# Kernel optimization log

Hardware: AMD Instinct MI355X
Metric: run time of the kernel (lower is better)

## Reference

```python
import jax, jax.numpy as jnp
import numpy as np

HIST_LEN = 100  # STDP history cap in the original module


def setup_inputs() -> dict:
    key = jax.random.key(0)
    ks = jax.random.split(key, 5)
    H, B = 1024, 16384
    return {
        "x": jax.random.normal(ks[0], (B, H), dtype=jnp.float32),
        "weights": jax.random.normal(ks[1], (H, H), dtype=jnp.float32) * 0.1,
        "meta_plasticity": jnp.ones((H,), dtype=jnp.float32),
        "pre_hist": jax.random.normal(ks[2], (HIST_LEN, H), dtype=jnp.float32) * 0.1,
        "post_hist": jax.random.normal(ks[3], (HIST_LEN, H), dtype=jnp.float32) * 0.1,
        "activity_history": jnp.zeros((1000,), dtype=jnp.float32),
        "history_pointer": 5,
        "stdp_window": jnp.float32(20.0),
        "stdp_decay": jnp.float32(0.1),
        "target_activity": jnp.float32(0.1),
        "homeostatic_rate": jnp.float32(0.01),
        "meta_learning_rate": jnp.float32(0.001),
    }


def reference(x, weights, meta_plasticity, pre_hist, post_hist,
              activity_history, history_pointer, stdp_window, stdp_decay,
              target_activity, homeostatic_rate, meta_learning_rate):
    # --- forward matmul: weights * meta_plasticity scales columns (broadcast over rows)
    output = x @ (weights * meta_plasticity)  # [B, H]

    # --- STDP update (vectorized form of the python loop over the history) ---
    # append current mean activities, pop oldest (steady-state length == HIST_LEN)
    pre = jnp.concatenate([pre_hist[1:], x.mean(axis=0)[None]], axis=0)       # [L, H]
    post = jnp.concatenate([post_hist[1:], output.mean(axis=0)[None]], axis=0)
    L = HIST_LEN
    i = jnp.arange(L, dtype=jnp.float32)
    dt = (L - i) * stdp_window
    w = 0.01 * jnp.exp(-dt * stdp_decay)                                      # [L]
    pos_w = jnp.where(i < L - 1, w, 0.0)   # i < len-1 branch
    neg_w = jnp.where(i > 0, w, 0.0)       # i > 0 branch
    # sum_i pos_w[i] * outer(post[-1], pre[i]) = outer(post[-1], pos_w @ pre)
    dW = jnp.outer(post[-1], pos_w @ pre) - jnp.outer(neg_w @ post, pre[-1])
    new_w = jnp.clip(weights + dW, -1.0, 1.0)

    # --- homeostatic plasticity ---
    hist = activity_history.at[history_pointer].set(output.mean())
    activity_diff = target_activity - hist.mean()
    new_w = jnp.clip(new_w * (1.0 + homeostatic_rate * activity_diff), -1.0, 1.0)

    # --- meta plasticity ---
    new_meta = jnp.clip(
        meta_plasticity + meta_learning_rate * (output.mean(axis=0) - meta_plasticity),
        0.0, 2.0)

    return output, new_w, new_meta, hist
```

## Files before the change

kernel.cpp:

```cpp
#include <hip/hip_runtime.h>
#include <hip/hip_bf16.h>

#define H 1024
#define BATCH 16384

typedef unsigned short u16;
typedef u16 u16x8 __attribute__((ext_vector_type(8)));
typedef __bf16 bf16x8 __attribute__((ext_vector_type(8)));
typedef float f32x4 __attribute__((ext_vector_type(4)));

typedef __attribute__((address_space(3))) unsigned int lds_uint;
typedef __attribute__((address_space(1))) const unsigned int glob_uint;

__device__ __forceinline__ u16 f2bf(float f) {
  unsigned int u = __float_as_uint(f);
  u += 0x7fffu + ((u >> 16) & 1u);
  return (u16)(u >> 16);
}

#define WS_XSUMP   0
#define WS_XSUM    (WS_XSUMP + 256 * H)
#define WS_ORAWP   (WS_XSUM + H)
#define WS_POSVP   (WS_ORAWP + 16 * H)
#define WS_NEGHP   (WS_POSVP + 5 * H)
#define WS_SCRATCH (WS_NEGHP + 5 * H)
#define WS_BF16    (WS_SCRATCH + 16)

__global__ __launch_bounds__(256) void prep_kernel(const float* __restrict__ X,
                                                   const float* __restrict__ W,
                                                   u16* __restrict__ Xb,
                                                   u16* __restrict__ Wbt,
                                                   float* __restrict__ ws,
                                                   const float* __restrict__ pre,
                                                   const float* __restrict__ post,
                                                   const float* __restrict__ win,
                                                   const float* __restrict__ dec) {
  __shared__ __align__(16) u16 t[64][72];
  const int b = blockIdx.x, tid = threadIdx.x;
  if (b < 256) {
    size_t r0 = (size_t)b * 64;
    float s0 = 0.f, s1 = 0.f, s2 = 0.f, s3 = 0.f;
#pragma unroll 4
    for (int r = 0; r < 64; ++r) {
      size_t off = (r0 + r) * H + tid * 4;
      const float4 v = *(const float4*)&X[off];
      ushort4 h;
      h.x = f2bf(v.x); h.y = f2bf(v.y); h.z = f2bf(v.z); h.w = f2bf(v.w);
      *(ushort4*)&Xb[off] = h;
      s0 += v.x; s1 += v.y; s2 += v.z; s3 += v.w;
    }
    float* row = &ws[WS_XSUMP + b * H];
    row[tid * 4 + 0] = s0; row[tid * 4 + 1] = s1;
    row[tid * 4 + 2] = s2; row[tid * 4 + 3] = s3;
  } else if (b < 512) {
    const int b2 = b - 256;
    const int n0 = (b2 & 15) * 64, k0 = (b2 >> 4) * 64;
    const int rb = tid >> 4, c4 = tid & 15;
#pragma unroll
    for (int i = 0; i < 4; ++i) {
      int r = rb + i * 16;
      const float4 v = *(const float4*)&W[(size_t)(k0 + r) * H + n0 + c4 * 4];
      t[c4 * 4 + 0][r] = f2bf(v.x);
      t[c4 * 4 + 1][r] = f2bf(v.y);
      t[c4 * 4 + 2][r] = f2bf(v.z);
      t[c4 * 4 + 3][r] = f2bf(v.w);
    }
    __syncthreads();
    const int seg = tid & 7;
#pragma unroll
    for (int p = 0; p < 2; ++p) {
      int wr = p * 32 + (tid >> 3);
      *(u16x8*)&Wbt[(size_t)(n0 + wr) * H + k0 + seg * 8] = *(const u16x8*)&t[wr][seg * 8];
    }
  } else {
    const int b2 = b - 512;
    const int col = (b2 & 3) * 256 + tid;
    const int seg = b2 >> 2;
    const int t0 = 1 + seg * 20;
    int tend = t0 + 20; if (tend > 100) tend = 100;
    float wd = win[0] * dec[0];
    float ps = 0.f, ns = 0.f;
    for (int tt = t0; tt < tend; ++tt) {
      float w = 0.01f * expf(-(float)(101 - tt) * wd);
      ps += w * pre[tt * H + col];
      if (tt >= 2) ns += w * post[tt * H + col];
    }
    ws[WS_POSVP + seg * H + col] = ps;
    ws[WS_NEGHP + seg * H + col] = ns;
  }
}

__global__ __launch_bounds__(256) void gemm_vm_kernel(const u16* __restrict__ Xb,
                                                      const u16* __restrict__ Wbt,
                                                      const float* __restrict__ meta,
                                                      const float* __restrict__ W,
                                                      float* __restrict__ ws,
                                                      float* __restrict__ out) {
  __shared__ __align__(16) u16 lA[128 * 32];
  __shared__ __align__(16) u16 lB[128 * 32];
  __shared__ float xs[64];

  const int b = blockIdx.x, tid = threadIdx.x;

  if (b < 64) {
    const int jx = b & 3, ky = b >> 2;
    if (tid < 64) {
      float s = 0.f;
      const float* p = &ws[WS_XSUMP + ky * 64 + tid];
#pragma unroll 8
      for (int q = 0; q < 256; ++q) s += p[q * H];
      xs[tid] = s;
      if (jx == 0) ws[WS_XSUM + ky * 64 + tid] = s;
    }
    __syncthreads();
    const int j = jx * 256 + tid;
    float s = 0.f;
#pragma unroll 8
    for (int k = 0; k < 64; ++k) s += xs[k] * W[(size_t)(ky * 64 + k) * H + j];
    ws[WS_ORAWP + ky * H + j] = s * (1.0f / (float)BATCH);
    return;
  }

  const int bg = b - 64;
  const int mt = bg & 127, nt = bg >> 7;
  const size_t row0 = (size_t)mt * 128;
  const int col0 = nt * 128;
  const int wave = tid >> 6;
  const int lane = tid & 63;
  const int quad = lane >> 4;
  const int l16 = lane & 15;
  const int wm = wave >> 1, wn = wave & 1;

  const int sr = lane >> 2;
  const int sk = (lane & 3) * 8;

  f32x4 acc[4][4];
#pragma unroll
  for (int i = 0; i < 4; ++i)
#pragma unroll
    for (int j = 0; j < 4; ++j) acc[i][j] = (f32x4){0.f, 0.f, 0.f, 0.f};

  for (int k0 = 0; k0 < H; k0 += 32) {
#pragma unroll
    for (int i = 0; i < 2; ++i) {
      const int rg = i * 64 + wave * 16;
      const u16* ga = &Xb[(row0 + rg + sr) * H + k0 + sk];
      const u16* gb = &Wbt[(size_t)(col0 + rg + sr) * H + k0 + sk];
      __builtin_amdgcn_global_load_lds((glob_uint*)ga, (lds_uint*)&lA[rg * 32], 16, 0, 0);
      __builtin_amdgcn_global_load_lds((glob_uint*)gb, (lds_uint*)&lB[rg * 32], 16, 0, 0);
    }
    __syncthreads();

    bf16x8 av[4], bv[4];
#pragma unroll
    for (int f = 0; f < 4; ++f) {
      av[f] = __builtin_bit_cast(bf16x8, *(const u16x8*)&lA[(wm * 64 + f * 16 + l16) * 32 + quad * 8]);
      bv[f] = __builtin_bit_cast(bf16x8, *(const u16x8*)&lB[(wn * 64 + f * 16 + l16) * 32 + quad * 8]);
    }
#pragma unroll
    for (int fm = 0; fm < 4; ++fm)
#pragma unroll
      for (int fn = 0; fn < 4; ++fn)
        acc[fm][fn] = __builtin_amdgcn_mfma_f32_16x16x32_bf16(av[fm], bv[fn], acc[fm][fn], 0, 0, 0);
    __syncthreads();
  }

  float mcol[4];
#pragma unroll
  for (int fn = 0; fn < 4; ++fn) mcol[fn] = meta[col0 + wn * 64 + fn * 16 + l16];
#pragma unroll
  for (int fm = 0; fm < 4; ++fm) {
#pragma unroll
    for (int fn = 0; fn < 4; ++fn) {
      int col = col0 + wn * 64 + fn * 16 + l16;
#pragma unroll
      for (int r = 0; r < 4; ++r) {
        size_t row = row0 + wm * 64 + fm * 16 + quad * 4 + r;
        out[row * H + col] = acc[fm][fn][r] * mcol[fn];
      }
    }
  }
}

__global__ __launch_bounds__(256) void tail_kernel(const float* __restrict__ W,
                                                   const float* __restrict__ meta,
                                                   const float* __restrict__ act,
                                                   const int* __restrict__ ptr,
                                                   const float* __restrict__ targ,
                                                   const float* __restrict__ homeo,
                                                   const float* __restrict__ mlr,
                                                   const float* __restrict__ win,
                                                   const float* __restrict__ dec,
                                                   const float* __restrict__ ws,
                                                   float* __restrict__ out_w,
                                                   float* __restrict__ meta_out,
                                                   float* __restrict__ hist_out) {
  __shared__ float r1[4], r2[4];
  const int r = blockIdx.x;
  const int t = threadIdx.x;
  const int c4 = t * 4;

  f32x4 oraw = (f32x4){0.f, 0.f, 0.f, 0.f};
#pragma unroll
  for (int i = 0; i < 16; ++i) {
    const float4 v = *(const float4*)&ws[WS_ORAWP + i * H + c4];
    oraw[0] += v.x; oraw[1] += v.y; oraw[2] += v.z; oraw[3] += v.w;
  }
  const float4 mv = *(const float4*)&meta[c4];
  f32x4 om;
  om[0] = mv.x * oraw[0]; om[1] = mv.y * oraw[1];
  om[2] = mv.z * oraw[2]; om[3] = mv.w * oraw[3];

  float s1 = om[0] + om[1] + om[2] + om[3];
  float s2 = 0.f;
#pragma unroll
  for (int j = 0; j < 4; ++j) {
    int idx = t + j * 256;
    if (idx < 1000) s2 += act[idx];
  }
#pragma unroll
  for (int o = 32; o > 0; o >>= 1) {
    s1 += __shfl_down(s1, o, 64);
    s2 += __shfl_down(s2, o, 64);
  }
  if ((t & 63) == 0) { r1[t >> 6] = s1; r2[t >> 6] = s2; }
  __syncthreads();
  const float ts1 = r1[0] + r1[1] + r1[2] + r1[3];
  const float ts2 = r2[0] + r2[1] + r2[2] + r2[3];
  const float total_mean = ts1 / (float)H;
  const int p = ptr[0];
  const float hist_mean = (ts2 - act[p] + total_mean) / 1000.f;
  const float scale = 1.f + homeo[0] * (targ[0] - hist_mean);
  const float w99 = 0.01f * expf(-win[0] * dec[0]);

  float oraw_r = 0.f;
#pragma unroll
  for (int i = 0; i < 16; ++i) oraw_r += ws[WS_ORAWP + i * H + r];
  const float om_r = meta[r] * oraw_r;
  float negh_r = 0.f;
#pragma unroll
  for (int i = 0; i < 5; ++i) negh_r += ws[WS_NEGHP + i * H + r];
  const float neg_r = negh_r + w99 * om_r;

  f32x4 pv = (f32x4){0.f, 0.f, 0.f, 0.f};
#pragma unroll
  for (int i = 0; i < 5; ++i) {
    const float4 v = *(const float4*)&ws[WS_POSVP + i * H + c4];
    pv[0] += v.x; pv[1] += v.y; pv[2] += v.z; pv[3] += v.w;
  }
  const float4 xv = *(const float4*)&ws[WS_XSUM + c4];
  float xx[4] = {xv.x, xv.y, xv.z, xv.w};
  const float4 wv = *(const float4*)&W[(size_t)r * H + c4];
  float wx[4] = {wv.x, wv.y, wv.z, wv.w};
  float4 o;
  float ox[4];
#pragma unroll
  for (int i = 0; i < 4; ++i) {
    float v = wx[i] + om_r * pv[i] - neg_r * (xx[i] * (1.0f / (float)BATCH));
    v = fminf(fmaxf(v, -1.f), 1.f);
    v = v * scale;
    ox[i] = fminf(fmaxf(v, -1.f), 1.f);
  }
  o.x = ox[0]; o.y = ox[1]; o.z = ox[2]; o.w = ox[3];
  *(float4*)&out_w[(size_t)r * H + c4] = o;

  if (r == 0) {
    float4 nm;
    float nx[4] = {mv.x, mv.y, mv.z, mv.w};
    float nr[4];
#pragma unroll
    for (int i = 0; i < 4; ++i) {
      float v = nx[i] + mlr[0] * (om[i] - nx[i]);
      nr[i] = fminf(fmaxf(v, 0.f), 2.f);
    }
    nm.x = nr[0]; nm.y = nr[1]; nm.z = nr[2]; nm.w = nr[3];
    *(float4*)&meta_out[c4] = nm;
#pragma unroll
    for (int j = 0; j < 4; ++j) {
      int idx = t + j * 256;
      if (idx < 1000) hist_out[idx] = (idx == p) ? total_mean : act[idx];
    }
  }
}

__global__ __launch_bounds__(256) void colsum_kernel(const float* __restrict__ x,
                                                     float* __restrict__ xsum) {
  int col = blockIdx.x * 256 + threadIdx.x;
  size_t r0 = (size_t)blockIdx.y * 256;
  float s = 0.f;
#pragma unroll 8
  for (int r = 0; r < 256; ++r) s += x[(r0 + r) * H + col];
  atomicAdd(&xsum[col], s);
}

__global__ __launch_bounds__(256) void gemm_fallback_kernel(const float* __restrict__ X,
                                                            const float* __restrict__ W,
                                                            const float* __restrict__ meta,
                                                            float* __restrict__ out) {
  __shared__ __align__(16) u16 lA[128][40];
  __shared__ __align__(16) u16 lB[128][40];
  const int tid = threadIdx.x;
  const int wave = tid >> 6;
  const int lane = tid & 63;
  const int quad = lane >> 4;
  const int l16 = lane & 15;
  const int wm = wave >> 1, wn = wave & 1;
  const size_t row0 = (size_t)blockIdx.x * 128;
  const int col0 = blockIdx.y * 128;
  f32x4 acc[4][4];
#pragma unroll
  for (int i = 0; i < 4; ++i)
#pragma unroll
    for (int j = 0; j < 4; ++j) acc[i][j] = (f32x4){0.f, 0.f, 0.f, 0.f};
  for (int k0 = 0; k0 < H; k0 += 32) {
#pragma unroll
    for (int i = 0; i < 4; ++i) {
      int idx = i * 256 + tid;
      int r = idx >> 3, c4 = idx & 7;
      const float4 v = *(const float4*)&X[(row0 + r) * H + k0 + c4 * 4];
      ushort4 h;
      h.x = f2bf(v.x); h.y = f2bf(v.y); h.z = f2bf(v.z); h.w = f2bf(v.w);
      *(ushort4*)&lA[r][c4 * 4] = h;
    }
#pragma unroll
    for (int i = 0; i < 4; ++i) {
      int idx = i * 256 + tid;
      int kk = idx >> 5, c4 = idx & 31;
      const float4 v = *(const float4*)&W[(size_t)(k0 + kk) * H + col0 + c4 * 4];
      lB[c4 * 4 + 0][kk] = f2bf(v.x);
      lB[c4 * 4 + 1][kk] = f2bf(v.y);
      lB[c4 * 4 + 2][kk] = f2bf(v.z);
      lB[c4 * 4 + 3][kk] = f2bf(v.w);
    }
    __syncthreads();
    bf16x8 av[4], bv[4];
#pragma unroll
    for (int f = 0; f < 4; ++f) {
      av[f] = __builtin_bit_cast(bf16x8, *(const u16x8*)&lA[wm * 64 + f * 16 + l16][quad * 8]);
      bv[f] = __builtin_bit_cast(bf16x8, *(const u16x8*)&lB[wn * 64 + f * 16 + l16][quad * 8]);
    }
#pragma unroll
    for (int fm = 0; fm < 4; ++fm)
#pragma unroll
      for (int fn = 0; fn < 4; ++fn)
        acc[fm][fn] = __builtin_amdgcn_mfma_f32_16x16x32_bf16(av[fm], bv[fn], acc[fm][fn], 0, 0, 0);
    __syncthreads();
  }
  float mcol[4];
#pragma unroll
  for (int fn = 0; fn < 4; ++fn) mcol[fn] = meta[col0 + wn * 64 + fn * 16 + l16];
#pragma unroll
  for (int fm = 0; fm < 4; ++fm) {
#pragma unroll
    for (int fn = 0; fn < 4; ++fn) {
      int col = col0 + wn * 64 + fn * 16 + l16;
#pragma unroll
      for (int r = 0; r < 4; ++r) {
        size_t row = row0 + wm * 64 + fm * 16 + quad * 4 + r;
        out[row * H + col] = acc[fm][fn][r] * mcol[fn];
      }
    }
  }
}

__global__ __launch_bounds__(256) void vecmat_kernel(const float* __restrict__ W,
                                                     const float* __restrict__ xsum,
                                                     float* __restrict__ outraw) {
  int j = blockIdx.x * 256 + threadIdx.x;
  int k0 = blockIdx.y * 64;
  float s = 0.f;
#pragma unroll 8
  for (int k = 0; k < 64; ++k) s += xsum[k0 + k] * W[(size_t)(k0 + k) * H + j];
  atomicAdd(&outraw[j], s * (1.0f / (float)BATCH));
}

__global__ __launch_bounds__(256) void stdpvec_kernel(const float* __restrict__ pre,
                                                      const float* __restrict__ post,
                                                      const float* __restrict__ win,
                                                      const float* __restrict__ dec,
                                                      float* __restrict__ posv,
                                                      float* __restrict__ negh) {
  int col = blockIdx.x * 256 + threadIdx.x;
  int t0 = 1 + blockIdx.y * 20;
  float wd = win[0] * dec[0];
  float ps = 0.f, ns = 0.f;
  int tend = t0 + 20;
  if (tend > 100) tend = 100;
  for (int t = t0; t < tend; ++t) {
    float w = 0.01f * expf(-(float)(101 - t) * wd);
    ps += w * pre[t * H + col];
    if (t >= 2) ns += w * post[t * H + col];
  }
  atomicAdd(&posv[col], ps);
  atomicAdd(&negh[col], ns);
}

__global__ __launch_bounds__(1024) void finalize_kernel(const float* __restrict__ meta,
                                                        const float* __restrict__ act,
                                                        const int* __restrict__ ptr,
                                                        const float* __restrict__ targ,
                                                        const float* __restrict__ homeo,
                                                        const float* __restrict__ mlr,
                                                        const float* __restrict__ outraw,
                                                        float* __restrict__ outmean,
                                                        float* __restrict__ scalep,
                                                        float* __restrict__ meta_out,
                                                        float* __restrict__ hist_out) {
  __shared__ float r1[16], r2[16];
  __shared__ float sc[2];
  int t = threadIdx.x;
  float om = meta[t] * outraw[t];
  outmean[t] = om;
  float a = (t < 1000) ? act[t] : 0.f;
  float s1 = om, s2 = a;
#pragma unroll
  for (int o = 32; o > 0; o >>= 1) {
    s1 += __shfl_down(s1, o, 64);
    s2 += __shfl_down(s2, o, 64);
  }
  if ((t & 63) == 0) { r1[t >> 6] = s1; r2[t >> 6] = s2; }
  __syncthreads();
  if (t == 0) {
    float ts1 = 0.f, ts2 = 0.f;
#pragma unroll
    for (int i = 0; i < 16; ++i) { ts1 += r1[i]; ts2 += r2[i]; }
    float total_mean = ts1 / (float)H;
    int p = ptr[0];
    float hist_mean = (ts2 - act[p] + total_mean) / 1000.f;
    float diff = targ[0] - hist_mean;
    sc[0] = 1.f + homeo[0] * diff;
    sc[1] = total_mean;
    scalep[0] = sc[0];
  }
  __syncthreads();
  float nm = meta[t] + mlr[0] * (om - meta[t]);
  nm = fminf(fmaxf(nm, 0.f), 2.f);
  meta_out[t] = nm;
  if (t < 1000) hist_out[t] = (t == ptr[0]) ? sc[1] : act[t];
}

__global__ __launch_bounds__(256) void neww_kernel(const float* __restrict__ W,
                                                   const float* __restrict__ outmean,
                                                   const float* __restrict__ posv,
                                                   const float* __restrict__ negh,
                                                   const float* __restrict__ xsum,
                                                   const float* __restrict__ scalep,
                                                   const float* __restrict__ win,
                                                   const float* __restrict__ dec,
                                                   float* __restrict__ out) {
  int idx4 = blockIdx.x * 256 + threadIdx.x;
  int rr = idx4 >> 8;
  int c4 = (idx4 & 255) * 4;
  float w99 = 0.01f * expf(-win[0] * dec[0]);
  float scale = scalep[0];
  float om_r = outmean[rr];
  float neg_r = negh[rr] + w99 * om_r;
  const float4 wv = *(const float4*)&W[(size_t)rr * H + c4];
  const float4 pv = *(const float4*)&posv[c4];
  const float4 xv = *(const float4*)&xsum[c4];
  float4 o;
  float vx[4] = {wv.x, wv.y, wv.z, wv.w};
  float px[4] = {pv.x, pv.y, pv.z, pv.w};
  float xx[4] = {xv.x, xv.y, xv.z, xv.w};
  float ox[4];
#pragma unroll
  for (int i = 0; i < 4; ++i) {
    float v = vx[i] + om_r * px[i] - neg_r * (xx[i] * (1.0f / (float)BATCH));
    v = fminf(fmaxf(v, -1.f), 1.f);
    v = v * scale;
    ox[i] = fminf(fmaxf(v, -1.f), 1.f);
  }
  o.x = ox[0]; o.y = ox[1]; o.z = ox[2]; o.w = ox[3];
  *(float4*)&out[(size_t)rr * H + c4] = o;
}

extern "C" void kernel_launch(void* const* d_in, const int* in_sizes, int n_in,
                              void* d_out, int out_size, void* d_ws, size_t ws_size,
                              hipStream_t stream) {
  const float* x     = (const float*)d_in[0];
  const float* W     = (const float*)d_in[1];
  const float* meta  = (const float*)d_in[2];
  const float* pre   = (const float*)d_in[3];
  const float* post  = (const float*)d_in[4];
  const float* act   = (const float*)d_in[5];
  const int*   ptr   = (const int*)d_in[6];
  const float* win   = (const float*)d_in[7];
  const float* dec   = (const float*)d_in[8];
  const float* targ  = (const float*)d_in[9];
  const float* homeo = (const float*)d_in[10];
  const float* mlr   = (const float*)d_in[11];

  float* out_y    = (float*)d_out;
  float* out_w    = out_y + (size_t)BATCH * H;
  float* out_meta = out_w + (size_t)H * H;
  float* out_hist = out_meta + H;

  float* ws = (float*)d_ws;
  u16* Xb  = (u16*)(ws + WS_BF16);
  u16* Wbt = Xb + (size_t)BATCH * H;

  const size_t ws_need = (size_t)WS_BF16 * sizeof(float) +
                         ((size_t)BATCH * H + (size_t)H * H) * sizeof(u16);

  if (ws_size >= ws_need) {
    prep_kernel<<<532, 256, 0, stream>>>(x, W, Xb, Wbt, ws, pre, post, win, dec);
    gemm_vm_kernel<<<1088, 256, 0, stream>>>(Xb, Wbt, meta, W, ws, out_y);
    tail_kernel<<<1024, 256, 0, stream>>>(W, meta, act, ptr, targ, homeo, mlr,
                                          win, dec, ws, out_w, out_meta, out_hist);
  } else {
    float* xsum    = ws;
    float* outraw  = ws + 1024;
    float* outmean = ws + 2048;
    float* posv    = ws + 3072;
    float* negh    = ws + 4096;
    float* scalep  = ws + 5120;
    hipMemsetAsync(d_ws, 0, 6144 * sizeof(float), stream);
    colsum_kernel<<<dim3(4, 64), 256, 0, stream>>>(x, xsum);
    gemm_fallback_kernel<<<dim3(128, 8), 256, 0, stream>>>(x, W, meta, out_y);
    vecmat_kernel<<<dim3(4, 16), 256, 0, stream>>>(W, xsum, outraw);
    stdpvec_kernel<<<dim3(4, 5), 256, 0, stream>>>(pre, post, win, dec, posv, negh);
    finalize_kernel<<<1, 1024, 0, stream>>>(meta, act, ptr, targ, homeo, mlr,
                                            outraw, outmean, scalep, out_meta, out_hist);
    neww_kernel<<<1024, 256, 0, stream>>>(W, outmean, posv, negh, xsum, scalep, win, dec, out_w);
  }
}
```

Measured before the change: 215.0 us.

## Double-buffer GEMM LDS tiles with XOR swizzle and MFMA priority boost

```diff
diff --git a/kernel.cpp b/kernel.cpp
--- a/kernel.cpp
+++ b/kernel.cpp
@@ -96,8 +96,8 @@
                                                       const float* __restrict__ W,
                                                       float* __restrict__ ws,
                                                       float* __restrict__ out) {
-  __shared__ __align__(16) u16 lA[128 * 32];
-  __shared__ __align__(16) u16 lB[128 * 32];
+  __shared__ __align__(16) u16 lA[2][128 * 32];
+  __shared__ __align__(16) u16 lB[2][128 * 32];
   __shared__ float xs[64];
 
   const int b = blockIdx.x, tid = threadIdx.x;
@@ -132,7 +132,8 @@
   const int wm = wave >> 1, wn = wave & 1;
 
   const int sr = lane >> 2;
-  const int sk = (lane & 3) * 8;
+  const int sk = (((lane & 3) ^ ((sr >> 1) & 3)) * 8);
+  const int ksw = ((quad ^ ((l16 >> 1) & 3)) * 8);
 
   f32x4 acc[4][4];
 #pragma unroll
@@ -140,29 +141,48 @@
 #pragma unroll
     for (int j = 0; j < 4; ++j) acc[i][j] = (f32x4){0.f, 0.f, 0.f, 0.f};
 
-  for (int k0 = 0; k0 < H; k0 += 32) {
-#pragma unroll
-    for (int i = 0; i < 2; ++i) {
-      const int rg = i * 64 + wave * 16;
-      const u16* ga = &Xb[(row0 + rg + sr) * H + k0 + sk];
-      const u16* gb = &Wbt[(size_t)(col0 + rg + sr) * H + k0 + sk];
-      __builtin_amdgcn_global_load_lds((glob_uint*)ga, (lds_uint*)&lA[rg * 32], 16, 0, 0);
-      __builtin_amdgcn_global_load_lds((glob_uint*)gb, (lds_uint*)&lB[rg * 32], 16, 0, 0);
-    }
-    __syncthreads();
+#pragma unroll
+  for (int i = 0; i < 2; ++i) {
+    const int rg = i * 64 + wave * 16;
+    const u16* ga = &Xb[(row0 + rg + sr) * H + 0 + sk];
+    const u16* gb = &Wbt[(size_t)(col0 + rg + sr) * H + 0 + sk];
+    __builtin_amdgcn_global_load_lds((glob_uint*)ga, (lds_uint*)&lA[0][rg * 32], 16, 0, 0);
+    __builtin_amdgcn_global_load_lds((glob_uint*)gb, (lds_uint*)&lB[0][rg * 32], 16, 0, 0);
+  }
+
+  for (int kt = 0; kt < 32; ++kt) {
+    const int cur = kt & 1;
+    if (kt < 31) {
+      const int k0n = (kt + 1) * 32;
+#pragma unroll
+      for (int i = 0; i < 2; ++i) {
+        const int rg = i * 64 + wave * 16;
+        const u16* ga = &Xb[(row0 + rg + sr) * H + k0n + sk];
+        const u16* gb = &Wbt[(size_t)(col0 + rg + sr) * H + k0n + sk];
+        __builtin_amdgcn_global_load_lds((glob_uint*)ga, (lds_uint*)&lA[cur ^ 1][rg * 32], 16, 0, 0);
+        __builtin_amdgcn_global_load_lds((glob_uint*)gb, (lds_uint*)&lB[cur ^ 1][rg * 32], 16, 0, 0);
+      }
+      asm volatile("s_waitcnt vmcnt(4)" ::: "memory");
+    } else {
+      asm volatile("s_waitcnt vmcnt(0)" ::: "memory");
+    }
+    asm volatile("s_barrier" ::: "memory");
 
     bf16x8 av[4], bv[4];
 #pragma unroll
     for (int f = 0; f < 4; ++f) {
-      av[f] = __builtin_bit_cast(bf16x8, *(const u16x8*)&lA[(wm * 64 + f * 16 + l16) * 32 + quad * 8]);
-      bv[f] = __builtin_bit_cast(bf16x8, *(const u16x8*)&lB[(wn * 64 + f * 16 + l16) * 32 + quad * 8]);
-    }
+      av[f] = __builtin_bit_cast(bf16x8, *(const u16x8*)&lA[cur][(wm * 64 + f * 16 + l16) * 32 + ksw]);
+      bv[f] = __builtin_bit_cast(bf16x8, *(const u16x8*)&lB[cur][(wn * 64 + f * 16 + l16) * 32 + ksw]);
+    }
+    __builtin_amdgcn_s_setprio(1);
 #pragma unroll
     for (int fm = 0; fm < 4; ++fm)
 #pragma unroll
       for (int fn = 0; fn < 4; ++fn)
         acc[fm][fn] = __builtin_amdgcn_mfma_f32_16x16x32_bf16(av[fm], bv[fn], acc[fm][fn], 0, 0, 0);
-    __syncthreads();
+    __builtin_amdgcn_s_setprio(0);
+    asm volatile("s_waitcnt lgkmcnt(0)" ::: "memory");
+    asm volatile("s_barrier" ::: "memory");
   }
 
   float mcol[4];
```

New measurement: 213.8 us. Within noise of the previous version (-0.6%).

## Rewrite GEMM as 256x256-tile, 8-wave kernel with multi-stage LDS pipeline

Applied to the files above, without the earlier changes.

```diff
diff --git a/kernel.cpp b/kernel.cpp
--- a/kernel.cpp
+++ b/kernel.cpp
@@ -90,19 +90,18 @@
   }
 }
 
-__global__ __launch_bounds__(256) void gemm_vm_kernel(const u16* __restrict__ Xb,
-                                                      const u16* __restrict__ Wbt,
-                                                      const float* __restrict__ meta,
-                                                      const float* __restrict__ W,
-                                                      float* __restrict__ ws,
-                                                      float* __restrict__ out) {
-  __shared__ __align__(16) u16 lA[128 * 32];
-  __shared__ __align__(16) u16 lB[128 * 32];
-  __shared__ float xs[64];
+__global__ __launch_bounds__(512, 2) void gemm_vm_kernel(const u16* __restrict__ Xb,
+                                                         const u16* __restrict__ Wbt,
+                                                         const float* __restrict__ meta,
+                                                         const float* __restrict__ W,
+                                                         float* __restrict__ ws,
+                                                         float* __restrict__ out) {
+  __shared__ __align__(16) u16 lds[65536];
 
   const int b = blockIdx.x, tid = threadIdx.x;
 
   if (b < 64) {
+    float* xs = (float*)lds;
     const int jx = b & 3, ky = b >> 2;
     if (tid < 64) {
       float s = 0.f;
@@ -113,69 +112,126 @@
       if (jx == 0) ws[WS_XSUM + ky * 64 + tid] = s;
     }
     __syncthreads();
-    const int j = jx * 256 + tid;
-    float s = 0.f;
+    if (tid < 256) {
+      const int j = jx * 256 + tid;
+      float s = 0.f;
 #pragma unroll 8
-    for (int k = 0; k < 64; ++k) s += xs[k] * W[(size_t)(ky * 64 + k) * H + j];
-    ws[WS_ORAWP + ky * H + j] = s * (1.0f / (float)BATCH);
+      for (int k = 0; k < 64; ++k) s += xs[k] * W[(size_t)(ky * 64 + k) * H + j];
+      ws[WS_ORAWP + ky * H + j] = s * (1.0f / (float)BATCH);
+    }
     return;
   }
 
   const int bg = b - 64;
-  const int mt = bg & 127, nt = bg >> 7;
-  const size_t row0 = (size_t)mt * 128;
-  const int col0 = nt * 128;
-  const int wave = tid >> 6;
-  const int lane = tid & 63;
-  const int quad = lane >> 4;
-  const int l16 = lane & 15;
-  const int wm = wave >> 1, wn = wave & 1;
-
-  const int sr = lane >> 2;
-  const int sk = (lane & 3) * 8;
-
-  f32x4 acc[4][4];
-#pragma unroll
-  for (int i = 0; i < 4; ++i)
+  const int mt = bg >> 2, nt = bg & 3;
+  const size_t row0 = (size_t)mt * 256;
+  const int col0 = nt * 256;
+  const int wid = tid >> 6, lane = tid & 63;
+  const int wm = wid >> 2, wn = wid & 3;
+  const int quad = lane >> 4, l16 = lane & 15;
+  const int xsw = l16 & 7;
+
+  const int srow = lane >> 3;
+  const int schunk = (lane & 7) ^ (srow & 7);
+
+  auto stageA = [&](int t, int h) {
+#pragma unroll
+    for (int s = 0; s < 2; ++s) {
+      const u16* ga = &Xb[(row0 + h * 128 + s * 64 + wid * 8 + srow) * H + t * 64 + schunk * 8];
+      lds_uint* ld = (lds_uint*)&lds[(((2 * t + h) & 3) * 8192) + s * 4096 + wid * 512];
+      __builtin_amdgcn_global_load_lds((glob_uint*)ga, ld, 16, 0, 0);
+    }
+  };
+  auto stageB = [&](int t, int h) {
+#pragma unroll
+    for (int s = 0; s < 2; ++s) {
+      const u16* gb = &Wbt[(size_t)(col0 + h * 128 + s * 64 + wid * 8 + srow) * H + t * 64 + schunk * 8];
+      lds_uint* ld = (lds_uint*)&lds[32768 + (((2 * t + h) & 3) * 8192) + s * 4096 + wid * 512];
+      __builtin_amdgcn_global_load_lds((glob_uint*)gb, ld, 16, 0, 0);
+    }
+  };
+
+  f32x4 acc[8][4];
+#pragma unroll
+  for (int i = 0; i < 8; ++i)
 #pragma unroll
     for (int j = 0; j < 4; ++j) acc[i][j] = (f32x4){0.f, 0.f, 0.f, 0.f};
 
-  for (int k0 = 0; k0 < H; k0 += 32) {
-#pragma unroll
-    for (int i = 0; i < 2; ++i) {
-      const int rg = i * 64 + wave * 16;
-      const u16* ga = &Xb[(row0 + rg + sr) * H + k0 + sk];
-      const u16* gb = &Wbt[(size_t)(col0 + rg + sr) * H + k0 + sk];
-      __builtin_amdgcn_global_load_lds((glob_uint*)ga, (lds_uint*)&lA[rg * 32], 16, 0, 0);
-      __builtin_amdgcn_global_load_lds((glob_uint*)gb, (lds_uint*)&lB[rg * 32], 16, 0, 0);
-    }
-    __syncthreads();
-
-    bf16x8 av[4], bv[4];
-#pragma unroll
-    for (int f = 0; f < 4; ++f) {
-      av[f] = __builtin_bit_cast(bf16x8, *(const u16x8*)&lA[(wm * 64 + f * 16 + l16) * 32 + quad * 8]);
-      bv[f] = __builtin_bit_cast(bf16x8, *(const u16x8*)&lB[(wn * 64 + f * 16 + l16) * 32 + quad * 8]);
-    }
-#pragma unroll
-    for (int fm = 0; fm < 4; ++fm)
-#pragma unroll
-      for (int fn = 0; fn < 4; ++fn)
-        acc[fm][fn] = __builtin_amdgcn_mfma_f32_16x16x32_bf16(av[fm], bv[fn], acc[fm][fn], 0, 0, 0);
-    __syncthreads();
+  stageA(0, 0); stageA(0, 1); stageB(0, 0); stageB(0, 1); stageB(1, 0); stageB(1, 1);
+  asm volatile("s_waitcnt vmcnt(4)" ::: "memory");
+  __builtin_amdgcn_s_barrier();
+
+  for (int it = 0; it < 8; ++it) {
+    const bool last = (it == 7);
+#pragma unroll
+    for (int hf = 0; hf < 2; ++hf) {
+      const int tc = 2 * it + hf;
+      const int aslot = ((2 * tc + wm) & 3) * 8192;
+      const int bslot = 32768 + ((2 * tc + (wn >> 1)) & 3) * 8192;
+      const int brl = (wn & 1) * 64;
+      bf16x8 bv[4][2];
+#pragma unroll
+      for (int sub = 0; sub < 4; ++sub) {
+        if (hf == 0) {
+          if (sub == 0)      stageA(2 * it + 1, 0);
+          else if (sub == 1) stageA(2 * it + 1, 1);
+          else if (sub == 2) { if (!last) stageB(2 * it + 2, 0); }
+          else               { if (!last) stageB(2 * it + 2, 1); }
+        } else {
+          if (sub == 0)      { if (!last) stageA(2 * it + 2, 0); }
+          else if (sub == 1) { if (!last) stageA(2 * it + 2, 1); }
+          else if (sub == 2) { if (!last) stageB(2 * it + 3, 0); }
+          else               { if (!last) stageB(2 * it + 3, 1); }
+        }
+        if (sub == 0) {
+#pragma unroll
+          for (int fn = 0; fn < 4; ++fn)
+#pragma unroll
+            for (int ks = 0; ks < 2; ++ks)
+              bv[fn][ks] = __builtin_bit_cast(bf16x8,
+                *(const u16x8*)&lds[bslot + (brl + fn * 16 + l16) * 64 + (((ks * 4 + quad) ^ xsw) * 8)]);
+        }
+        bf16x8 av[2][2];
+#pragma unroll
+        for (int fi = 0; fi < 2; ++fi)
+#pragma unroll
+          for (int ks = 0; ks < 2; ++ks)
+            av[fi][ks] = __builtin_bit_cast(bf16x8,
+              *(const u16x8*)&lds[aslot + ((sub * 2 + fi) * 16 + l16) * 64 + (((ks * 4 + quad) ^ xsw) * 8)]);
+
+        __builtin_amdgcn_s_barrier();
+        asm volatile("s_waitcnt lgkmcnt(0)" ::: "memory");
+        __builtin_amdgcn_sched_barrier(0);
+        __builtin_amdgcn_s_setprio(1);
+#pragma unroll
+        for (int fi = 0; fi < 2; ++fi)
+#pragma unroll
+          for (int fn = 0; fn < 4; ++fn)
+#pragma unroll
+            for (int ks = 0; ks < 2; ++ks)
+              acc[sub * 2 + fi][fn] = __builtin_amdgcn_mfma_f32_16x16x32_bf16(
+                  av[fi][ks], bv[fn][ks], acc[sub * 2 + fi][fn], 0, 0, 0);
+        __builtin_amdgcn_s_setprio(0);
+        if (sub == 3) {
+          if (hf == 0 && last) asm volatile("s_waitcnt vmcnt(0)" ::: "memory");
+          else                 asm volatile("s_waitcnt vmcnt(4)" ::: "memory");
+        }
+        __builtin_amdgcn_s_barrier();
+      }
+    }
   }
 
   float mcol[4];
 #pragma unroll
   for (int fn = 0; fn < 4; ++fn) mcol[fn] = meta[col0 + wn * 64 + fn * 16 + l16];
 #pragma unroll
-  for (int fm = 0; fm < 4; ++fm) {
+  for (int fm = 0; fm < 8; ++fm) {
 #pragma unroll
     for (int fn = 0; fn < 4; ++fn) {
-      int col = col0 + wn * 64 + fn * 16 + l16;
+      const int col = col0 + wn * 64 + fn * 16 + l16;
 #pragma unroll
       for (int r = 0; r < 4; ++r) {
-        size_t row = row0 + wm * 64 + fm * 16 + quad * 4 + r;
+        size_t row = row0 + wm * 128 + fm * 16 + quad * 4 + r;
         out[row * H + col] = acc[fm][fn][r] * mcol[fn];
       }
     }
@@ -504,7 +560,7 @@
 
   if (ws_size >= ws_need) {
     prep_kernel<<<532, 256, 0, stream>>>(x, W, Xb, Wbt, ws, pre, post, win, dec);
-    gemm_vm_kernel<<<1088, 256, 0, stream>>>(Xb, Wbt, meta, W, ws, out_y);
+    gemm_vm_kernel<<<320, 512, 0, stream>>>(Xb, Wbt, meta, W, ws, out_y);
     tail_kernel<<<1024, 256, 0, stream>>>(W, meta, act, ptr, targ, homeo, mlr,
                                           win, dec, ws, out_w, out_meta, out_hist);
   } else {
```

After: 202.7 us. 5.8% less time.
